# Performance work log

Hardware: AMD Instinct MI355X
Metric: run time of the kernel (lower is better)

The kernel has to match this reference:

```python
import jax, jax.numpy as jnp
import numpy as np

B, D, F, P = 65536, 256, 512, 256


def setup_inputs() -> dict:
    key = jax.random.key(0)
    k_x, k_f, k_p, k_a, k_b, k_t = jax.random.split(key, 6)
    x = jax.random.normal(k_x, (B, D), dtype=jnp.float32)
    # reset_parameters: uniform(-0.27, 1)
    features = jax.random.uniform(k_f, (F, D), dtype=jnp.float32, minval=-0.27, maxval=1.0)
    prototypes = jax.random.uniform(k_p, (P, D), dtype=jnp.float32, minval=-0.27, maxval=1.0)
    # alpha/beta/theta init to zeros in the module; use small random values so the
    # output is non-trivial for kernel correctness checking.
    alpha = jax.random.normal(k_a, (1,), dtype=jnp.float32) * 0.1
    beta = jax.random.normal(k_b, (1,), dtype=jnp.float32) * 0.1
    theta = jax.random.normal(k_t, (1,), dtype=jnp.float32) * 0.1
    return {"x": x, "features": features, "prototypes": prototypes,
            "alpha": alpha, "beta": beta, "theta": theta}


def reference(x, features, prototypes, alpha, beta, theta):
    # Shared projections
    x_features = x @ features.T                 # [B, F]
    p_features = prototypes @ features.T        # [P, F]
    x_present = jax.nn.relu(x_features)         # [B, F]
    p_present = jax.nn.relu(p_features)         # [P, F]
    x_weighted = x_features * x_present         # [B, F]
    p_weighted = p_features * p_present         # [P, F]

    # Tversky terms
    common = x_weighted @ p_weighted.T                          # [B, P]
    x_weighted_sum = jnp.sum(x_weighted, axis=1, keepdims=True)  # [B, 1]
    x_p_interaction = x_weighted @ p_present.T                  # [B, P]
    x_distinctive = x_weighted_sum - x_p_interaction            # [B, P]
    p_weighted_sum = jnp.sum(p_weighted, axis=1)[None, :]        # [1, P]
    x_p_weighted_interaction = x_present @ p_weighted.T         # [B, P]
    p_distinctive = p_weighted_sum - x_p_weighted_interaction   # [B, P]

    return theta * common - alpha * x_distinctive - beta * p_distinctive
```

## Files before the change

### kernel.cpp

```cpp
#include <hip/hip_runtime.h>
#include <cstdint>
#include <cstddef>

#define Bsz 65536
#define Dsz 256
#define Fsz 512
#define Psz 256

typedef __attribute__((ext_vector_type(8))) short short8;
typedef __attribute__((ext_vector_type(4))) short short4v;
typedef __attribute__((ext_vector_type(4))) float float4v;
typedef __attribute__((ext_vector_type(16))) float float16v;

__device__ inline short f2bf(float f) {
    unsigned u = __builtin_bit_cast(unsigned, f);
    u = (u + 0x7FFFu + ((u >> 16) & 1u)) >> 16;
    return (short)u;
}
__device__ inline float bf2f(short s) {
    unsigned u = ((unsigned)(unsigned short)s) << 16;
    return __builtin_bit_cast(float, u);
}


__global__ void k_prep(const float* __restrict__ features, short* __restrict__ featbB,
                       float* __restrict__ pws_neg) {
    int idx = blockIdx.x * 256 + threadIdx.x;
    int f = idx >> 5, d0 = (idx & 31) * 8;
    float4v v0 = *(const float4v*)(features + (size_t)f * Dsz + d0);
    float4v v1 = *(const float4v*)(features + (size_t)f * Dsz + d0 + 4);
    short8 s;
    s[0] = f2bf(v0.x); s[1] = f2bf(v0.y); s[2] = f2bf(v0.z); s[3] = f2bf(v0.w);
    s[4] = f2bf(v1.x); s[5] = f2bf(v1.y); s[6] = f2bf(v1.z); s[7] = f2bf(v1.w);
    int lane = (f & 15) + 16 * ((d0 >> 3) & 3);
    size_t o = (size_t)(f >> 4) * 4096 + (size_t)(d0 >> 5) * 512 + (size_t)lane * 8;
    *(short8*)&featbB[o] = s;
    if (idx < Psz) pws_neg[idx] = 0.f;
}

#define SBPITCH 136

__global__ __launch_bounds__(256, 2) void k_pside(
    const float* __restrict__ prototypes, const short* __restrict__ featbB,
    const float* __restrict__ beta_p,
    short* __restrict__ pwB, short* __restrict__ pmB, float* __restrict__ pws_neg)
{
    __shared__ char lds[35840];
    short* As = (short*)lds;
    short* Sb = (short*)lds;

    const int t = threadIdx.x;
    const int w = t >> 6, lane = t & 63, l15 = lane & 15, l4 = lane >> 4;
    const int rowg = blockIdx.x >> 2, nc = blockIdx.x & 3;
    const float beta = *beta_p;

    float4v acc[4][4];
    #pragma unroll
    for (int a = 0; a < 4; ++a)
        #pragma unroll
        for (int b = 0; b < 4; ++b) acc[a][b] = (float4v){0.f, 0.f, 0.f, 0.f};

    const float* pbase = prototypes + (size_t)rowg * 128 * Dsz;

    for (int kc = 0; kc < 4; ++kc) {
        __syncthreads();
        #pragma unroll
        for (int j = 0; j < 8; ++j) {
            int idx = j * 1024 + t * 4;
            int r = idx >> 6, c = idx & 63;
            float4v v = *(const float4v*)(pbase + (size_t)r * Dsz + kc * 64 + c);
            int unit = r * 8 + ((c >> 3) ^ (r & 7));
            short4v s; s.x = f2bf(v.x); s.y = f2bf(v.y); s.z = f2bf(v.z); s.w = f2bf(v.w);
            *(short4v*)((char*)As + unit * 16 + (c & 7) * 2) = s;
        }
        __syncthreads();
        #pragma unroll
        for (int kk = 0; kk < 2; ++kk) {
            short8 af[4], bf[4];
            const int k8 = kk * 4 + l4;
            #pragma unroll
            for (int tm = 0; tm < 4; ++tm) {
                int m = (w & 1) * 64 + tm * 16 + l15;
                af[tm] = *(const short8*)&As[(m * 8 + (k8 ^ (m & 7))) * 8];
            }
            #pragma unroll
            for (int tn = 0; tn < 4; ++tn) {
                int fcb = nc * 8 + (w >> 1) * 4 + tn;
                bf[tn] = *(const short8*)&featbB[(size_t)fcb * 4096 +
                                                 (size_t)(kc * 2 + kk) * 512 + (size_t)lane * 8];
            }
            #pragma unroll
            for (int tm = 0; tm < 4; ++tm)
                #pragma unroll
                for (int tn = 0; tn < 4; ++tn)
                    acc[tm][tn] = __builtin_amdgcn_mfma_f32_16x16x32_bf16(af[tm], bf[tn], acc[tm][tn], 0, 0, 0);
        }
    }
    __syncthreads();
    #pragma unroll
    for (int tm = 0; tm < 4; ++tm)
        #pragma unroll
        for (int tn = 0; tn < 4; ++tn)
            #pragma unroll
            for (int r = 0; r < 4; ++r) {
                int row = (w & 1) * 64 + tm * 16 + l4 * 4 + r;
                int col = (w >> 1) * 64 + tn * 16 + l15;
                Sb[row * SBPITCH + col] = f2bf(acc[tm][tn][r]);
            }
    __syncthreads();
    #pragma unroll
    for (int rep = 0; rep < 8; ++rep) {
        int u = rep * 256 + t;
        int row = u >> 4, i = u & 15;
        short8 sv = *(const short8*)&Sb[row * SBPITCH + i * 8];
        short8 pwv, pmv;
        float sum = 0.f;
        #pragma unroll
        for (int e = 0; e < 8; ++e) {
            float pf = bf2f(sv[e]);
            float pp = fmaxf(pf, 0.f);
            float pw = pf * pp;
            pwv[e] = f2bf(pw);
            pmv[e] = f2bf(pp - 1.0f);
            sum += pw;
        }
        int p = rowg * 128 + row;
        int gcol = nc * 128 + i * 8;
        size_t fo = (size_t)(gcol >> 4) * 4096 + (size_t)(p >> 6) * 1024 +
                    (size_t)((p >> 5) & 1) * 512 +
                    (size_t)((p & 31) + 32 * ((gcol >> 3) & 1)) * 8;
        *(short8*)&pwB[fo] = pwv;
        *(short8*)&pmB[fo] = pmv;
        #pragma unroll
        for (int mk = 1; mk < 16; mk <<= 1) sum += __shfl_xor(sum, mk, 64);
        if ((lane & 15) == 0) atomicAdd(&pws_neg[p], -beta * sum);
    }
}

__global__ __launch_bounds__(256, 3) void k_main(
    const float* __restrict__ x, const short* __restrict__ featbB,
    const short* __restrict__ pwB, const short* __restrict__ pmB,
    const float* __restrict__ pws_neg,
    const float* __restrict__ alpha_p, const float* __restrict__ beta_p,
    const float* __restrict__ theta_p, float* __restrict__ out)
{
    __shared__ short A12[4096];

    const int t = threadIdx.x;
    const int w = t >> 6, lane = t & 63, l15 = lane & 15, l4 = lane >> 4;
    const int l31 = lane & 31, half = lane >> 5;
    const float alpha = *alpha_p, beta = *beta_p, theta = *theta_p;
    const size_t row0 = (size_t)blockIdx.x * 64;

    short8 xreg[8];
    {
        const float* xr = x + (row0 + 16 * w + l15) * Dsz + l4 * 8;
        #pragma unroll
        for (int kk = 0; kk < 8; ++kk) {
            float4v v0 = *(const float4v*)(xr + kk * 32);
            float4v v1 = *(const float4v*)(xr + kk * 32 + 4);
            short8 s;
            s[0] = f2bf(v0.x); s[1] = f2bf(v0.y); s[2] = f2bf(v0.z); s[3] = f2bf(v0.w);
            s[4] = f2bf(v1.x); s[5] = f2bf(v1.y); s[6] = f2bf(v1.z); s[7] = f2bf(v1.w);
            xreg[kk] = s;
        }
    }

    float16v acc[2][2];
    #pragma unroll
    for (int a = 0; a < 2; ++a)
        #pragma unroll
        for (int b = 0; b < 2; ++b)
            #pragma unroll
            for (int e = 0; e < 16; ++e) acc[a][b][e] = 0.f;

    const int mbase = 16 * w + l4 * 4;

    for (int fc = 0; fc < 32; ++fc) {
        const int buf = (fc & 1) << 11;

        const short* fbase = featbB + (size_t)fc * 4096 + (size_t)lane * 8;
        float4v s0 = (float4v){0.f, 0.f, 0.f, 0.f};
        float4v s1 = (float4v){0.f, 0.f, 0.f, 0.f};
        #pragma unroll
        for (int kk = 0; kk < 8; kk += 2) {
            short8 b0 = *(const short8*)(fbase + kk * 512);
            short8 b1 = *(const short8*)(fbase + kk * 512 + 512);
            s0 = __builtin_amdgcn_mfma_f32_16x16x32_bf16(xreg[kk],     b0, s0, 0, 0, 0);
            s1 = __builtin_amdgcn_mfma_f32_16x16x32_bf16(xreg[kk + 1], b1, s1, 0, 0, 0);
        }

        #pragma unroll
        for (int r = 0; r < 4; ++r) {
            float sv = s0[r] + s1[r];
            float xp = fmaxf(sv, 0.f);
            float xw = sv * xp;
            int m = mbase + r;
            int swz = (m >> 2) & 3;
            int u1 = m * 4 + ((l15 >> 3) ^ swz);
            int u2 = m * 4 + ((2 | (l15 >> 3)) ^ swz);
            A12[buf + u1 * 8 + (l15 & 7)] = f2bf(theta * xw + beta * xp);
            A12[buf + u2 * 8 + (l15 & 7)] = f2bf(alpha * xw);
        }

        const short* pb = pwB + (size_t)fc * 4096 + (size_t)w * 1024 + (size_t)lane * 8;
        const short* mb = pmB + (size_t)fc * 4096 + (size_t)w * 1024 + (size_t)lane * 8;
        short8 bw0 = *(const short8*)(pb);
        short8 bw1 = *(const short8*)(pb + 512);
        short8 bm0 = *(const short8*)(mb);
        short8 bm1 = *(const short8*)(mb + 512);

        __syncthreads();

        short8 a1f[2], a2f[2];
        #pragma unroll
        for (int mi = 0; mi < 2; ++mi) {
            int m = 32 * mi + l31;
            int swz = (m >> 2) & 3;
            a1f[mi] = *(const short8*)&A12[buf + (m * 4 + (half ^ swz)) * 8];
            a2f[mi] = *(const short8*)&A12[buf + (m * 4 + ((2 | half) ^ swz)) * 8];
        }
        #pragma unroll
        for (int mi = 0; mi < 2; ++mi) {
            acc[mi][0] = __builtin_amdgcn_mfma_f32_32x32x16_bf16(a1f[mi], bw0, acc[mi][0], 0, 0, 0);
            acc[mi][0] = __builtin_amdgcn_mfma_f32_32x32x16_bf16(a2f[mi], bm0, acc[mi][0], 0, 0, 0);
            acc[mi][1] = __builtin_amdgcn_mfma_f32_32x32x16_bf16(a1f[mi], bw1, acc[mi][1], 0, 0, 0);
            acc[mi][1] = __builtin_amdgcn_mfma_f32_32x32x16_bf16(a2f[mi], bm1, acc[mi][1], 0, 0, 0);
        }
    }

    #pragma unroll
    for (int ni = 0; ni < 2; ++ni) {
        int col = 64 * w + 32 * ni + l31;
        float pn = pws_neg[col];
        #pragma unroll
        for (int mi = 0; mi < 2; ++mi)
            #pragma unroll
            for (int rg = 0; rg < 16; ++rg) {
                size_t grow = row0 + 32 * mi + (rg & 3) + 8 * (rg >> 2) + 4 * half;
                out[grow * Psz + col] = acc[mi][ni][rg] + pn;
            }
    }
}

extern "C" void kernel_launch(void* const* d_in, const int* in_sizes, int n_in,
                              void* d_out, int out_size, void* d_ws, size_t ws_size,
                              hipStream_t stream) {
    const float* x          = (const float*)d_in[0];
    const float* features   = (const float*)d_in[1];
    const float* prototypes = (const float*)d_in[2];
    const float* alpha      = (const float*)d_in[3];
    const float* beta       = (const float*)d_in[4];
    const float* theta      = (const float*)d_in[5];
    float* out = (float*)d_out;

    char* ws = (char*)d_ws;
    short* featbB  = (short*)(ws);
    short* pwB     = (short*)(ws + 262144);
    short* pmB     = (short*)(ws + 524288);
    float* pws_neg = (float*)(ws + 786432);

    hipLaunchKernelGGL(k_prep,  dim3(64),   dim3(256), 0, stream, features, featbB, pws_neg);
    hipLaunchKernelGGL(k_pside, dim3(8),    dim3(256), 0, stream, prototypes, featbB, beta,
                       pwB, pmB, pws_neg);
    hipLaunchKernelGGL(k_main,  dim3(1024), dim3(256), 0, stream, x, featbB, pwB, pmB,
                       pws_neg, alpha, beta, theta, out);
}
```

Measured before the change: 194.8 us.

## Split output columns across two blocks and prefetch next-chunk operands in registers

Each 64-row group is now handled by two blocks, each computing 128 of the 256 prototype columns, so each wave keeps a single 32-column accumulator tile. The x-feature projection is recomputed in both blocks, adding redundant MFMA work. Feature and prototype fragments for the next F-chunk are loaded into double-buffered registers during the current chunk to hide global load latency. The grid doubles, trading extra compute for more parallelism and lower register pressure.

```diff
diff --git a/kernel.cpp b/kernel.cpp
--- a/kernel.cpp
+++ b/kernel.cpp
@@ -126,8 +126,7 @@
         }
         int p = rowg * 128 + row;
         int gcol = nc * 128 + i * 8;
-        size_t fo = (size_t)(gcol >> 4) * 4096 + (size_t)(p >> 6) * 1024 +
-                    (size_t)((p >> 5) & 1) * 512 +
+        size_t fo = (size_t)(gcol >> 4) * 4096 + (size_t)(p >> 5) * 512 +
                     (size_t)((p & 31) + 32 * ((gcol >> 3) & 1)) * 8;
         *(short8*)&pwB[fo] = pwv;
         *(short8*)&pmB[fo] = pmv;
@@ -149,8 +148,10 @@
     const int t = threadIdx.x;
     const int w = t >> 6, lane = t & 63, l15 = lane & 15, l4 = lane >> 4;
     const int l31 = lane & 31, half = lane >> 5;
+    const int rowg = blockIdx.x >> 1, ch = blockIdx.x & 1;
+    const int ntile = ch * 4 + w;
     const float alpha = *alpha_p, beta = *beta_p, theta = *theta_p;
-    const size_t row0 = (size_t)blockIdx.x * 64;
+    const size_t row0 = (size_t)rowg * 64;
 
     short8 xreg[8];
     {
@@ -166,29 +167,41 @@
         }
     }
 
-    float16v acc[2][2];
+    float16v acc[2];
     #pragma unroll
     for (int a = 0; a < 2; ++a)
         #pragma unroll
-        for (int b = 0; b < 2; ++b)
-            #pragma unroll
-            for (int e = 0; e < 16; ++e) acc[a][b][e] = 0.f;
+        for (int e = 0; e < 16; ++e) acc[a][e] = 0.f;
 
     const int mbase = 16 * w + l4 * 4;
-
-    for (int fc = 0; fc < 32; ++fc) {
+    const size_t lane8 = (size_t)lane * 8;
+
+    short8 fbA[8], fbB[8], pA[2], pB[2];
+
+    #pragma unroll
+    for (int kk = 0; kk < 8; ++kk)
+        fbA[kk] = *(const short8*)(featbB + kk * 512 + lane8);
+    pA[0] = *(const short8*)(pwB + (size_t)ntile * 512 + lane8);
+    pA[1] = *(const short8*)(pmB + (size_t)ntile * 512 + lane8);
+
+    auto body = [&](int fc, short8 (&fbc)[8], short8 (&fbn)[8],
+                    short8 (&pc)[2], short8 (&pn)[2]) {
         const int buf = (fc & 1) << 11;
-
-        const short* fbase = featbB + (size_t)fc * 4096 + (size_t)lane * 8;
+        const int fcn = (fc + 1) & 31;
+        const short* fbsrc = featbB + (size_t)fcn * 4096 + lane8;
+
         float4v s0 = (float4v){0.f, 0.f, 0.f, 0.f};
         float4v s1 = (float4v){0.f, 0.f, 0.f, 0.f};
         #pragma unroll
         for (int kk = 0; kk < 8; kk += 2) {
-            short8 b0 = *(const short8*)(fbase + kk * 512);
-            short8 b1 = *(const short8*)(fbase + kk * 512 + 512);
-            s0 = __builtin_amdgcn_mfma_f32_16x16x32_bf16(xreg[kk],     b0, s0, 0, 0, 0);
-            s1 = __builtin_amdgcn_mfma_f32_16x16x32_bf16(xreg[kk + 1], b1, s1, 0, 0, 0);
-        }
+            s0 = __builtin_amdgcn_mfma_f32_16x16x32_bf16(xreg[kk],     fbc[kk],     s0, 0, 0, 0);
+            s1 = __builtin_amdgcn_mfma_f32_16x16x32_bf16(xreg[kk + 1], fbc[kk + 1], s1, 0, 0, 0);
+        }
+
+        #pragma unroll
+        for (int kk = 0; kk < 4; ++kk) fbn[kk] = *(const short8*)(fbsrc + kk * 512);
+        pn[0] = *(const short8*)(pwB + (size_t)fcn * 4096 + (size_t)ntile * 512 + lane8);
+        pn[1] = *(const short8*)(pmB + (size_t)fcn * 4096 + (size_t)ntile * 512 + lane8);
 
         #pragma unroll
         for (int r = 0; r < 4; ++r) {
@@ -197,48 +210,40 @@
             float xw = sv * xp;
             int m = mbase + r;
             int swz = (m >> 2) & 3;
-            int u1 = m * 4 + ((l15 >> 3) ^ swz);
-            int u2 = m * 4 + ((2 | (l15 >> 3)) ^ swz);
-            A12[buf + u1 * 8 + (l15 & 7)] = f2bf(theta * xw + beta * xp);
-            A12[buf + u2 * 8 + (l15 & 7)] = f2bf(alpha * xw);
-        }
-
-        const short* pb = pwB + (size_t)fc * 4096 + (size_t)w * 1024 + (size_t)lane * 8;
-        const short* mb = pmB + (size_t)fc * 4096 + (size_t)w * 1024 + (size_t)lane * 8;
-        short8 bw0 = *(const short8*)(pb);
-        short8 bw1 = *(const short8*)(pb + 512);
-        short8 bm0 = *(const short8*)(mb);
-        short8 bm1 = *(const short8*)(mb + 512);
-
+            A12[buf + (m * 4 + ((l15 >> 3) ^ swz)) * 8 + (l15 & 7)]       = f2bf(theta * xw + beta * xp);
+            A12[buf + (m * 4 + ((2 | (l15 >> 3)) ^ swz)) * 8 + (l15 & 7)] = f2bf(alpha * xw);
+        }
         __syncthreads();
 
-        short8 a1f[2], a2f[2];
+        #pragma unroll
+        for (int kk = 4; kk < 8; ++kk) fbn[kk] = *(const short8*)(fbsrc + kk * 512);
+
         #pragma unroll
         for (int mi = 0; mi < 2; ++mi) {
             int m = 32 * mi + l31;
             int swz = (m >> 2) & 3;
-            a1f[mi] = *(const short8*)&A12[buf + (m * 4 + (half ^ swz)) * 8];
-            a2f[mi] = *(const short8*)&A12[buf + (m * 4 + ((2 | half) ^ swz)) * 8];
-        }
-        #pragma unroll
-        for (int mi = 0; mi < 2; ++mi) {
-            acc[mi][0] = __builtin_amdgcn_mfma_f32_32x32x16_bf16(a1f[mi], bw0, acc[mi][0], 0, 0, 0);
-            acc[mi][0] = __builtin_amdgcn_mfma_f32_32x32x16_bf16(a2f[mi], bm0, acc[mi][0], 0, 0, 0);
-            acc[mi][1] = __builtin_amdgcn_mfma_f32_32x32x16_bf16(a1f[mi], bw1, acc[mi][1], 0, 0, 0);
-            acc[mi][1] = __builtin_amdgcn_mfma_f32_32x32x16_bf16(a2f[mi], bm1, acc[mi][1], 0, 0, 0);
-        }
-    }
-
-    #pragma unroll
-    for (int ni = 0; ni < 2; ++ni) {
-        int col = 64 * w + 32 * ni + l31;
-        float pn = pws_neg[col];
+            short8 a1 = *(const short8*)&A12[buf + (m * 4 + (half ^ swz)) * 8];
+            short8 a2 = *(const short8*)&A12[buf + (m * 4 + ((2 | half) ^ swz)) * 8];
+            acc[mi] = __builtin_amdgcn_mfma_f32_32x32x16_bf16(a1, pc[0], acc[mi], 0, 0, 0);
+            acc[mi] = __builtin_amdgcn_mfma_f32_32x32x16_bf16(a2, pc[1], acc[mi], 0, 0, 0);
+        }
+    };
+
+    #pragma unroll 1
+    for (int fc = 0; fc < 32; fc += 2) {
+        body(fc,     fbA, fbB, pA, pB);
+        body(fc + 1, fbB, fbA, pB, pA);
+    }
+
+    {
+        int col = ntile * 32 + l31;
+        float pn_ = pws_neg[col];
         #pragma unroll
         for (int mi = 0; mi < 2; ++mi)
             #pragma unroll
             for (int rg = 0; rg < 16; ++rg) {
                 size_t grow = row0 + 32 * mi + (rg & 3) + 8 * (rg >> 2) + 4 * half;
-                out[grow * Psz + col] = acc[mi][ni][rg] + pn;
+                out[grow * Psz + col] = acc[mi][rg] + pn_;
             }
     }
 }
@@ -263,6 +268,6 @@
     hipLaunchKernelGGL(k_prep,  dim3(64),   dim3(256), 0, stream, features, featbB, pws_neg);
     hipLaunchKernelGGL(k_pside, dim3(8),    dim3(256), 0, stream, prototypes, featbB, beta,
                        pwB, pmB, pws_neg);
-    hipLaunchKernelGGL(k_main,  dim3(1024), dim3(256), 0, stream, x, featbB, pwB, pmB,
+    hipLaunchKernelGGL(k_main,  dim3(2048), dim3(256), 0, stream, x, featbB, pwB, pmB,
                        pws_neg, alpha, beta, theta, out);
 }
```

Measured after the change: 223.2 us. 1.15x slower.
